# Kernel tuning notes

Measured on AMD Instinct MI355X. Metric: run time of the kernel, lower is better.

The kernel has to match this reference:

```python
import jax, jax.numpy as jnp
import numpy as np

BLOCK_SIZE = 16
MASK_TOKEN_ID = 31999
D_MODEL = 2048
N_HEADS = 16
VOCAB = 32000
NEG = -1e30


def setup_inputs() -> dict:
    key = jax.random.key(0)
    ks = jax.random.split(key, 8)
    B, S, D, V = 1, 1024, D_MODEL, VOCAB
    sd = 1.0 / np.sqrt(D)
    return {
        "input_ids": jax.random.randint(ks[0], (B, S), 0, V),
        "attention_mask": jnp.ones((B, S), dtype=jnp.float32),
        "hidden_states": jax.random.normal(ks[1], (B, S, D), dtype=jnp.float32),
        "loss_mask": jnp.ones((B, S), dtype=jnp.float32),
        "embed_table": jax.random.normal(ks[2], (V, D), dtype=jnp.float32) * 0.02,
        "Wq": jax.random.normal(ks[3], (D, D), dtype=jnp.float32) * sd,
        "Wk": jax.random.normal(ks[4], (D, D), dtype=jnp.float32) * sd,
        "Wv": jax.random.normal(ks[5], (D, D), dtype=jnp.float32) * sd,
        "Wo": jax.random.normal(ks[6], (D, D), dtype=jnp.float32) * sd,
        "lm_head_w": jax.random.normal(ks[7], (D, V), dtype=jnp.float32) * sd,
    }


def reference(input_ids, attention_mask, hidden_states, loss_mask,
              embed_table, Wq, Wk, Wv, Wo, lm_head_w):
    B, S = input_ids.shape
    bs = BLOCK_SIZE
    L = (S // bs) * bs  # effective_len
    input_ids = input_ids[:, :L]
    hidden_states = hidden_states[:, :L, :]
    loss_mask = loss_mask[:, :L]

    positions = jnp.arange(L)
    is_block_start = positions % bs == 0
    block_ids = positions // bs

    # noise input: first token of each block real, rest MASK
    noise_ids = jnp.where(is_block_start[None, :], input_ids, MASK_TOKEN_ID)
    noise_emb = embed_table[noise_ids]  # [B, L, D]

    # [L, 2L] DFlash mask: ctx kv visible if its block < q block; noise kv if same block
    ctx_vis = block_ids[None, :] < block_ids[:, None]
    noise_vis = block_ids[:, None] == block_ids[None, :]
    full_mask = jnp.concatenate([ctx_vis, noise_vis], axis=1)  # [L, 2L] bool

    # draft attention: q from noise tokens, kv over [target_hidden ; noise]
    H = N_HEADS
    hd = hidden_states.shape[-1] // H
    kv_in = jnp.concatenate([hidden_states, noise_emb], axis=1)  # [B, 2L, D]
    q = (noise_emb @ Wq).reshape(B, L, H, hd).transpose(0, 2, 1, 3)      # [B,H,L,hd]
    k = (kv_in @ Wk).reshape(B, 2 * L, H, hd).transpose(0, 2, 1, 3)      # [B,H,2L,hd]
    v = (kv_in @ Wv).reshape(B, 2 * L, H, hd).transpose(0, 2, 1, 3)
    scores = jnp.einsum("bhqd,bhkd->bhqk", q, k) / jnp.sqrt(jnp.float32(hd))
    scores = jnp.where(full_mask[None, None, :, :], scores, NEG)
    attn = jax.nn.softmax(scores, axis=-1)
    ctx = jnp.einsum("bhqk,bhkd->bhqd", attn, v)
    hidden = ctx.transpose(0, 2, 1, 3).reshape(B, L, -1) @ Wo  # [B, L, D]

    logits = hidden @ lm_head_w  # [B, L, V]

    # dflash loss mask: exclude first block and block starts (gamma=None)
    is_first_block = block_ids == 0
    valid = (~is_first_block) & (~is_block_start)
    combined = loss_mask * valid.astype(jnp.float32)  # [B, L]
    active = combined > 1e-6

    logp = jax.nn.log_softmax(logits, axis=-1)
    ce = -jnp.take_along_axis(logp, input_ids[..., None], axis=-1)[..., 0]  # [B, L]
    count = jnp.sum(active.astype(jnp.float32))
    loss = jnp.sum(jnp.where(active, ce, 0.0)) / count

    preds = jnp.argmax(logits, axis=-1)
    correct = jnp.sum(jnp.where(active, (preds == input_ids).astype(jnp.float32), 0.0))
    accuracy = correct / count
    return loss, accuracy
```

## Files before the change

### kernel.cpp

```cpp
#include <hip/hip_runtime.h>

typedef unsigned int uint32;
typedef unsigned short u16;
typedef __attribute__((ext_vector_type(8))) short bf16x8;
typedef __attribute__((ext_vector_type(4))) float f32x4;

__device__ __forceinline__ u16 f2b(float f) {
  uint32 u = __float_as_uint(f);
  u = (u + 0x7fffu + ((u >> 16) & 1u)) >> 16;
  return (u16)u;
}
__device__ __forceinline__ float b2f(u16 h) {
  return __uint_as_float(((uint32)h) << 16);
}
__device__ __forceinline__ void gl_lds16(const void* g, void* l) {
  typedef const __attribute__((address_space(1))) void* gp_t;
  typedef __attribute__((address_space(3))) void* lp_t;
  __builtin_amdgcn_global_load_lds((gp_t)g, (lp_t)l, 16, 0, 0);
}

#define L 1024
#define D 2048
#define NH 16
#define HD 128
#define VOCAB 32000
#define KV 2048
#define MASK_ID 31999

static constexpr long OFF_KV  = 0;
static constexpr long OFF_WTQ = OFF_KV  + 8388608;
static constexpr long OFF_WTK = OFF_WTQ + 8388608;
static constexpr long OFF_WTV = OFF_WTK + 8388608;
static constexpr long OFF_WTO = OFF_WTV + 8388608;
static constexpr long OFF_Q   = OFF_WTO + 8388608;
static constexpr long OFF_K   = OFF_Q   + 4194304;
static constexpr long OFF_VT  = OFF_K   + 8388608;
static constexpr long OFF_SC  = OFF_VT  + 8388608;
static constexpr long OFF_CTX = OFF_SC  + 67108864;
static constexpr long OFF_HID = OFF_CTX + 4194304;
static constexpr long OFF_LMT = OFF_HID + 4194304;
static constexpr long OFF_LOG = OFF_LMT + 131072000;
static constexpr long OFF_ROW = OFF_LOG + 65536000;
static constexpr long WS_NEED = OFF_ROW + 8192;

__global__ __launch_bounds__(256) void prep_kv(const float* __restrict__ hs,
                                               const int* __restrict__ ids,
                                               const float* __restrict__ emb,
                                               u16* __restrict__ kv) {
  int r = blockIdx.x;
  int t = threadIdx.x;
  const float* src;
  if (r < L) {
    src = hs + (long)r * D;
  } else {
    int p = r - L;
    int id = ((p & 15) == 0) ? ids[p] : MASK_ID;
    src = emb + (long)id * D;
  }
  float4 a = *(const float4*)(src + t * 8);
  float4 b = *(const float4*)(src + t * 8 + 4);
  u16* dst = kv + (long)r * D + t * 8;
  ushort4 o0, o1;
  o0.x = f2b(a.x); o0.y = f2b(a.y); o0.z = f2b(a.z); o0.w = f2b(a.w);
  o1.x = f2b(b.x); o1.y = f2b(b.y); o1.z = f2b(b.z); o1.w = f2b(b.w);
  *(ushort4*)dst = o0;
  *(ushort4*)(dst + 4) = o1;
}

__device__ __forceinline__ void transpose_body(const float* __restrict__ W,
                                               u16* __restrict__ WT,
                                               int Kd, int Nd) {
  __shared__ float tile[64][65];
  int n0 = blockIdx.x * 64;
  int k0 = blockIdx.y * 64;
  int t = threadIdx.x;
#pragma unroll
  for (int p = 0; p < 4; ++p) {
    int idx = p * 256 + t;
    int r = idx >> 4;
    int c = (idx & 15) << 2;
    float4 v = *(const float4*)(W + (long)(k0 + r) * Nd + n0 + c);
    tile[r][c] = v.x; tile[r][c + 1] = v.y; tile[r][c + 2] = v.z; tile[r][c + 3] = v.w;
  }
  __syncthreads();
#pragma unroll
  for (int p = 0; p < 4; ++p) {
    int idx = p * 256 + t;
    int rn = idx >> 4;
    int ck = (idx & 15) << 2;
    ushort4 o;
    o.x = f2b(tile[ck][rn]);
    o.y = f2b(tile[ck + 1][rn]);
    o.z = f2b(tile[ck + 2][rn]);
    o.w = f2b(tile[ck + 3][rn]);
    *(ushort4*)(WT + (long)(n0 + rn) * Kd + k0 + ck) = o;
  }
}

__global__ __launch_bounds__(256) void transpose_conv(const float* __restrict__ W,
                                                      u16* __restrict__ WT,
                                                      int Kd, int Nd) {
  transpose_body(W, WT, Kd, Nd);
}

__global__ __launch_bounds__(256) void transpose4(const float* __restrict__ W0, const float* __restrict__ W1,
                                                  const float* __restrict__ W2, const float* __restrict__ W3,
                                                  u16* __restrict__ T0, u16* __restrict__ T1,
                                                  u16* __restrict__ T2, u16* __restrict__ T3) {
  int z = blockIdx.z;
  const float* W = (z == 0) ? W0 : (z == 1) ? W1 : (z == 2) ? W2 : W3;
  u16* T = (z == 0) ? T0 : (z == 1) ? T1 : (z == 2) ? T2 : T3;
  transpose_body(W, T, D, D);
}

#define EPI_PLAIN 0
#define EPI_QKV 3

template <int EPI>
__global__ __launch_bounds__(256) void gemm128(const u16* __restrict__ A, int lda, long aHead,
                                               const u16* __restrict__ BT, int ldb, long bHead,
                                               u16* __restrict__ C, int ldc, long cHead,
                                               int Kd) {
  __shared__ __align__(16) char lds[16384];
  char* a_lds = lds;
  char* b_lds = lds + 8192;
  int tid = threadIdx.x;
  int lane = tid & 63;
  int wave = tid >> 6;
  int wr = wave >> 1, wc = wave & 1;
  int h = blockIdx.z;
  long tm = (long)blockIdx.x * 128;
  long tn = (long)blockIdx.y * 128;
  const u16* Ap = A + (long)h * aHead + tm * lda;
  const u16* Bp = BT + (long)h * bHead + tn * ldb;

  int soff = tid * 16;
  int srow = soff >> 6;
  int scol = (soff & 63) >> 1;
  char* aldsb = a_lds + wave * 1024;
  char* bldsb = b_lds + wave * 1024;

  f32x4 acc[4][4];
#pragma unroll
  for (int i = 0; i < 4; ++i)
#pragma unroll
    for (int j = 0; j < 4; ++j) acc[i][j] = (f32x4){0.f, 0.f, 0.f, 0.f};

  for (int k0 = 0; k0 < Kd; k0 += 32) {
#pragma unroll
    for (int r = 0; r < 2; ++r) {
      gl_lds16(Ap + (long)(srow + r * 64) * lda + k0 + scol, aldsb + r * 4096);
      gl_lds16(Bp + (long)(srow + r * 64) * ldb + k0 + scol, bldsb + r * 4096);
    }
    __syncthreads();
    bf16x8 af[4], bfr[4];
    int ka = (lane >> 4) << 4;
#pragma unroll
    for (int mi = 0; mi < 4; ++mi)
      af[mi] = *(const bf16x8*)(a_lds + (wr * 64 + mi * 16 + (lane & 15)) * 64 + ka);
#pragma unroll
    for (int ni = 0; ni < 4; ++ni)
      bfr[ni] = *(const bf16x8*)(b_lds + (wc * 64 + ni * 16 + (lane & 15)) * 64 + ka);
#pragma unroll
    for (int mi = 0; mi < 4; ++mi)
#pragma unroll
      for (int ni = 0; ni < 4; ++ni)
        acc[mi][ni] = __builtin_amdgcn_mfma_f32_16x16x32_bf16(af[mi], bfr[ni], acc[mi][ni], 0, 0, 0);
    __syncthreads();
  }

  long crow0 = tm + wr * 64 + ((lane >> 4) << 2);
  int ccol0 = wc * 64 + (lane & 15);
  u16* Cp = C + (long)h * cHead;
#pragma unroll
  for (int mi = 0; mi < 4; ++mi) {
#pragma unroll
    for (int ni = 0; ni < 4; ++ni) {
      long col = tn + ccol0 + ni * 16;
#pragma unroll
      for (int j = 0; j < 4; ++j) {
        long row = crow0 + mi * 16 + j;
        Cp[row * ldc + col] = f2b(acc[mi][ni][j]);
      }
    }
  }
}

template <int EPI>
__global__ __launch_bounds__(512, 2) void gemm256(const u16* __restrict__ A, int lda,
                                                  const u16* __restrict__ BT, int ldb,
                                                  u16* __restrict__ C, int ldc,
                                                  int Kd, int mtiles,
                                                  u16* __restrict__ Cq, u16* __restrict__ Ck,
                                                  u16* __restrict__ Cv) {
  __shared__ __align__(16) char lds[131072];
  int nwg = gridDim.x;
  int orig = blockIdx.x;
  int q8 = nwg >> 3, r8 = nwg & 7;
  int xcd = orig & 7, idx = orig >> 3;
  int wg = (xcd < r8 ? xcd * (q8 + 1) : r8 * (q8 + 1) + (xcd - r8) * q8) + idx;
  int tm, tn;
  if (EPI == EPI_QKV) {
    if (wg < 32) { tn = wg >> 2; tm = 4 + (wg & 3); }
    else { int e = wg - 32; tn = 8 + (e >> 3); tm = e & 7; }
  } else {
    tm = wg % mtiles; tn = wg / mtiles;
  }

  int tid = threadIdx.x, lane = tid & 63, w = tid >> 6;
  int wm = w >> 2, wn = w & 3;
  const u16* Ap = A + (long)tm * 256 * lda;
  const u16* Bp = BT + (long)tn * 256 * ldb;
  int NT = Kd >> 6;
  int maxs = NT << 2;

  auto STAGE_SLOT = [&](int s) {
    if (s >= maxs) return;
    int tau = s >> 2, hh = s & 3;
    int kind = (hh & 1) ^ 1;
    int ks = hh >> 1;
    const u16* src = kind ? Bp : Ap;
    int ld = kind ? ldb : lda;
    char* dst0 = lds + (tau & 1) * 65536 + kind * 32768 + ks * 16384;
    long kbase = (long)tau * 64 + ks * 32;
#pragma unroll
    for (int l = 0; l < 2; ++l) {
      int o = tid * 16 + l * 8192;
      int rr = o >> 6;
      int ch = (o >> 4) & 3;
      int clog = ch ^ ((rr >> 1) & 3);
      gl_lds16(src + (long)rr * ld + kbase + clog * 8, dst0 + w * 1024 + l * 8192);
    }
  };
  auto LDA = [&](int tau, int ks, int mi) -> bf16x8 {
    int rr = wm * 128 + mi * 16 + (lane & 15);
    int qq = lane >> 4;
    return *(const bf16x8*)(lds + (tau & 1) * 65536 + ks * 16384 + rr * 64 +
                            ((qq ^ ((rr >> 1) & 3)) << 4));
  };
  auto LDB = [&](int tau, int ks, int ni) -> bf16x8 {
    int rr = wn * 64 + ni * 16 + (lane & 15);
    int qq = lane >> 4;
    return *(const bf16x8*)(lds + (tau & 1) * 65536 + 32768 + ks * 16384 + rr * 64 +
                            ((qq ^ ((rr >> 1) & 3)) << 4));
  };

  f32x4 acc[8][4];
#pragma unroll
  for (int i = 0; i < 8; ++i)
#pragma unroll
    for (int j = 0; j < 4; ++j) acc[i][j] = (f32x4){0.f, 0.f, 0.f, 0.f};

  STAGE_SLOT(0); STAGE_SLOT(1); STAGE_SLOT(2); STAGE_SLOT(3);
  asm volatile("s_waitcnt vmcnt(4)" ::: "memory");
  STAGE_SLOT(4); STAGE_SLOT(5); STAGE_SLOT(6);
  asm volatile("s_waitcnt vmcnt(6)" ::: "memory");
  __builtin_amdgcn_s_barrier();
  __builtin_amdgcn_sched_barrier(0);

  bf16x8 bfr[4];

#define G256_PHASE(TAU, KS, MH, SLOT, WAITV)                                   \
  {                                                                            \
    bf16x8 af[4];                                                              \
    if (MH == 0) {                                                             \
      bfr[0] = LDB(TAU, KS, 0); bfr[1] = LDB(TAU, KS, 1);                      \
      bfr[2] = LDB(TAU, KS, 2); bfr[3] = LDB(TAU, KS, 3);                      \
    }                                                                          \
    af[0] = LDA(TAU, KS, MH * 4 + 0); af[1] = LDA(TAU, KS, MH * 4 + 1);        \
    af[2] = LDA(TAU, KS, MH * 4 + 2); af[3] = LDA(TAU, KS, MH * 4 + 3);        \
    STAGE_SLOT(SLOT);                                                          \
    __builtin_amdgcn_sched_barrier(0);                                         \
    __builtin_amdgcn_s_barrier();                                              \
    asm volatile("s_waitcnt lgkmcnt(0)" ::: "memory");                         \
    __builtin_amdgcn_sched_barrier(0);                                         \
    __builtin_amdgcn_s_setprio(1);                                             \
    _Pragma("unroll")                                                          \
    for (int mi2 = 0; mi2 < 4; ++mi2)                                          \
      _Pragma("unroll")                                                        \
      for (int ni = 0; ni < 4; ++ni)                                           \
        acc[MH * 4 + mi2][ni] = __builtin_amdgcn_mfma_f32_16x16x32_bf16(       \
            af[mi2], bfr[ni], acc[MH * 4 + mi2][ni], 0, 0, 0);                 \
    __builtin_amdgcn_s_setprio(0);                                             \
    __builtin_amdgcn_sched_barrier(0);                                         \
    if (WAITV == 6) asm volatile("s_waitcnt vmcnt(6)" ::: "memory");           \
    else if (WAITV == 0) asm volatile("s_waitcnt vmcnt(0)" ::: "memory");      \
    __builtin_amdgcn_s_barrier();                                              \
    __builtin_amdgcn_sched_barrier(0);                                         \
  }

  for (int t = 0; t < NT; t += 2) {
    int s0 = 4 * t;
    int w4 = (t + 2 >= NT) ? 0 : 6;
    G256_PHASE(t,     0, 0, s0 + 7,  -1)
    G256_PHASE(t,     0, 1, s0 + 8,  -1)
    G256_PHASE(t,     1, 0, s0 + 9,  -1)
    G256_PHASE(t,     1, 1, s0 + 10, w4)
    G256_PHASE(t + 1, 0, 0, s0 + 11, -1)
    G256_PHASE(t + 1, 0, 1, s0 + 12, -1)
    G256_PHASE(t + 1, 1, 0, s0 + 13, -1)
    G256_PHASE(t + 1, 1, 1, s0 + 14, 6)
  }
#undef G256_PHASE

  long crow = (long)tm * 256 + wm * 128 + ((lane >> 4) << 2);
  long ccol = (long)tn * 256 + wn * 64 + (lane & 15);
#pragma unroll
  for (int mi = 0; mi < 8; ++mi)
#pragma unroll
    for (int ni = 0; ni < 4; ++ni)
#pragma unroll
      for (int j = 0; j < 4; ++j) {
        long row = crow + mi * 16 + j;
        long col = ccol + ni * 16;
        u16 val = f2b(acc[mi][ni][j]);
        if (EPI == EPI_PLAIN) {
          C[row * ldc + col] = val;
        } else {
          if (col < 2048) {
            if (row >= 1024) Cq[(row - 1024) * D + col] = val;
          } else if (col < 4096) {
            Ck[row * D + (col - 2048)] = val;
          } else {
            Cv[(col - 4096) * KV + row] = val;
          }
        }
      }
}

__global__ __launch_bounds__(256) void flash_attn(const u16* __restrict__ qb,
                                                  const u16* __restrict__ kb,
                                                  const u16* __restrict__ vt,
                                                  u16* __restrict__ ctx) {
  int tid = threadIdx.x;
  int lane = tid & 63;
  int wid = blockIdx.x * 4 + (tid >> 6);
  int h = wid >> 6;
  int rb = wid & 63;
  int lq = lane & 15;
  int g = lane >> 4;
  const float scale = 0.08838834764831845f;

  const u16* qrow = qb + (long)(rb * 16 + lq) * D + h * HD + g * 8;
  bf16x8 qf[4];
#pragma unroll
  for (int c = 0; c < 4; ++c) qf[c] = *(const bf16x8*)(qrow + c * 32);

  f32x4 o[8];
#pragma unroll
  for (int i = 0; i < 8; ++i) o[i] = (f32x4){0.f, 0.f, 0.f, 0.f};
  float m = -1e30f, lsum = 0.f;

  int nb = rb + 1;
  for (int bp = 0; bp < nb; bp += 2) {
    bool validB = (bp + 1) < nb;
    int tokA = (bp < rb) ? bp * 16 : 1024 + rb * 16;
    int bB = bp + 1;
    int tokB = validB ? ((bB < rb) ? bB * 16 : 1024 + rb * 16) : tokA;

    f32x4 sA = (f32x4){0.f, 0.f, 0.f, 0.f};
    f32x4 sB = (f32x4){0.f, 0.f, 0.f, 0.f};
    const u16* ka = kb + (long)(tokA + lq) * D + h * HD + g * 8;
#pragma unroll
    for (int c = 0; c < 4; ++c) {
      bf16x8 kf = *(const bf16x8*)(ka + c * 32);
      sA = __builtin_amdgcn_mfma_f32_16x16x32_bf16(kf, qf[c], sA, 0, 0, 0);
    }
    if (validB) {
      const u16* kbp = kb + (long)(tokB + lq) * D + h * HD + g * 8;
#pragma unroll
      for (int c = 0; c < 4; ++c) {
        bf16x8 kf = *(const bf16x8*)(kbp + c * 32);
        sB = __builtin_amdgcn_mfma_f32_16x16x32_bf16(kf, qf[c], sB, 0, 0, 0);
      }
    }

    float s8[8];
#pragma unroll
    for (int j = 0; j < 4; ++j) s8[j] = sA[j] * scale;
#pragma unroll
    for (int j = 0; j < 4; ++j) s8[4 + j] = validB ? sB[j] * scale : -1e30f;
    float mx = s8[0];
#pragma unroll
    for (int j = 1; j < 8; ++j) mx = fmaxf(mx, s8[j]);
    mx = fmaxf(mx, __shfl_xor(mx, 16));
    mx = fmaxf(mx, __shfl_xor(mx, 32));
    float mn = fmaxf(m, mx);
    float sc_f = __expf(m - mn);
    m = mn;
    float p[8], ps = 0.f;
#pragma unroll
    for (int j = 0; j < 8; ++j) { p[j] = __expf(s8[j] - mn); ps += p[j]; }
    ps += __shfl_xor(ps, 16);
    ps += __shfl_xor(ps, 32);
    lsum = lsum * sc_f + ps;

    uint32 Aw0 = (uint32)f2b(p[0]) | ((uint32)f2b(p[1]) << 16);
    uint32 Aw1 = (uint32)f2b(p[2]) | ((uint32)f2b(p[3]) << 16);
    uint32 Bw0 = (uint32)f2b(p[4]) | ((uint32)f2b(p[5]) << 16);
    uint32 Bw1 = (uint32)f2b(p[6]) | ((uint32)f2b(p[7]) << 16);
    int s0 = (((2 * g) & 3) << 4) + lq;
    int s1 = (((2 * g + 1) & 3) << 4) + lq;
    uint32 a00 = (uint32)__shfl((int)Aw0, s0), a01 = (uint32)__shfl((int)Aw1, s0);
    uint32 a10 = (uint32)__shfl((int)Aw0, s1), a11 = (uint32)__shfl((int)Aw1, s1);
    uint32 b00 = (uint32)__shfl((int)Bw0, s0), b01 = (uint32)__shfl((int)Bw1, s0);
    uint32 b10 = (uint32)__shfl((int)Bw0, s1), b11 = (uint32)__shfl((int)Bw1, s1);
    union { uint32 u[4]; bf16x8 v; } pu;
    pu.u[0] = (g < 2) ? a00 : b00;
    pu.u[1] = (g < 2) ? a01 : b01;
    pu.u[2] = (g < 2) ? a10 : b10;
    pu.u[3] = (g < 2) ? a11 : b11;

#pragma unroll
    for (int nt = 0; nt < 8; ++nt)
#pragma unroll
      for (int j = 0; j < 4; ++j) o[nt][j] *= sc_f;
    int tok_g = (g < 2) ? (tokA + g * 8) : (tokB + (g - 2) * 8);
    const u16* vrow = vt + (long)(h * HD + lq) * KV + tok_g;
#pragma unroll
    for (int nt = 0; nt < 8; ++nt) {
      bf16x8 vf = *(const bf16x8*)(vrow + (long)nt * 16 * KV);
      o[nt] = __builtin_amdgcn_mfma_f32_16x16x32_bf16(vf, pu.v, o[nt], 0, 0, 0);
    }
  }

  float inv = 1.f / lsum;
  u16* cp = ctx + (long)(rb * 16 + lq) * D + h * HD + g * 4;
#pragma unroll
  for (int nt = 0; nt < 8; ++nt) {
    ushort4 st;
    st.x = f2b(o[nt][0] * inv); st.y = f2b(o[nt][1] * inv);
    st.z = f2b(o[nt][2] * inv); st.w = f2b(o[nt][3] * inv);
    *(ushort4*)(cp + nt * 16) = st;
  }
}

__global__ __launch_bounds__(256) void row_ce(const u16* __restrict__ logits,
                                              const int* __restrict__ ids,
                                              float* __restrict__ rowbuf) {
  int row = blockIdx.x;
  const u16* p = logits + (long)row * VOCAB;
  int t = threadIdx.x;
  int lane = t & 63, w = t >> 6;
  float m = -1e30f;
  int am = VOCAB;
  for (int i = t * 8; i < VOCAB; i += 2048) {
    bf16x8 v = *(const bf16x8*)(p + i);
#pragma unroll
    for (int j = 0; j < 8; ++j) {
      float f = b2f((u16)v[j]);
      if (f > m) { m = f; am = i + j; }
      else if (f == m && (i + j) < am) am = i + j;
    }
  }
  for (int off = 1; off < 64; off <<= 1) {
    float om = __shfl_xor(m, off);
    int oa = __shfl_xor(am, off);
    if (om > m || (om == m && oa < am)) { m = om; am = oa; }
  }
  __shared__ float smax[4]; __shared__ int sidx[4]; __shared__ float ssum[4];
  if (lane == 0) { smax[w] = m; sidx[w] = am; }
  __syncthreads();
  float gm = smax[0]; int gi = sidx[0];
#pragma unroll
  for (int q = 1; q < 4; ++q) {
    if (smax[q] > gm || (smax[q] == gm && sidx[q] < gi)) { gm = smax[q]; gi = sidx[q]; }
  }
  float s = 0.f;
  for (int i = t * 8; i < VOCAB; i += 2048) {
    bf16x8 v = *(const bf16x8*)(p + i);
#pragma unroll
    for (int j = 0; j < 8; ++j) s += __expf(b2f((u16)v[j]) - gm);
  }
  for (int off = 1; off < 64; off <<= 1) s += __shfl_xor(s, off);
  if (lane == 0) ssum[w] = s;
  __syncthreads();
  if (t == 0) {
    float gs = ssum[0] + ssum[1] + ssum[2] + ssum[3];
    int tgt = ids[row];
    float tl = b2f(p[tgt]);
    rowbuf[row * 2] = gm + logf(gs) - tl;
    rowbuf[row * 2 + 1] = (gi == tgt) ? 1.f : 0.f;
  }
}

__global__ __launch_bounds__(256) void final_reduce(const float* __restrict__ rowbuf,
                                                    const float* __restrict__ loss_mask,
                                                    float* __restrict__ out) {
  int t = threadIdx.x;
  float ce = 0.f, cnt = 0.f, cor = 0.f;
  for (int r = t; r < L; r += 256) {
    bool valid = (r >= 16) && ((r & 15) != 0);
    float comb = loss_mask[r] * (valid ? 1.f : 0.f);
    if (comb > 1e-6f) {
      ce += rowbuf[r * 2];
      cor += rowbuf[r * 2 + 1];
      cnt += 1.f;
    }
  }
  for (int off = 1; off < 64; off <<= 1) {
    ce += __shfl_xor(ce, off);
    cnt += __shfl_xor(cnt, off);
    cor += __shfl_xor(cor, off);
  }
  __shared__ float s1[4], s2[4], s3[4];
  int lane = t & 63, w = t >> 6;
  if (lane == 0) { s1[w] = ce; s2[w] = cnt; s3[w] = cor; }
  __syncthreads();
  if (t == 0) {
    float C = s1[0] + s1[1] + s1[2] + s1[3];
    float N = s2[0] + s2[1] + s2[2] + s2[3];
    float R = s3[0] + s3[1] + s3[2] + s3[3];
    out[0] = C / N;
    out[1] = R / N;
  }
}

__global__ void ws_too_small(float* out, float mb) {
  if (threadIdx.x == 0) { out[0] = 1e6f + mb; out[1] = -1e6f; }
}

extern "C" void kernel_launch(void* const* d_in, const int* in_sizes, int n_in,
                              void* d_out, int out_size, void* d_ws, size_t ws_size,
                              hipStream_t stream) {
  const int* ids = (const int*)d_in[0];
  const float* hs = (const float*)d_in[2];
  const float* lmask = (const float*)d_in[3];
  const float* emb = (const float*)d_in[4];
  const float* Wq = (const float*)d_in[5];
  const float* Wk = (const float*)d_in[6];
  const float* Wv = (const float*)d_in[7];
  const float* Wo = (const float*)d_in[8];
  const float* Wlm = (const float*)d_in[9];
  float* out = (float*)d_out;
  char* ws = (char*)d_ws;

  if (ws_size < (size_t)WS_NEED) {
    ws_too_small<<<1, 64, 0, stream>>>(out, (float)(ws_size >> 20));
    return;
  }

  u16* kv  = (u16*)(ws + OFF_KV);
  u16* wtq = (u16*)(ws + OFF_WTQ);
  u16* wtk = (u16*)(ws + OFF_WTK);
  u16* wtv = (u16*)(ws + OFF_WTV);
  u16* wto = (u16*)(ws + OFF_WTO);
  u16* qb  = (u16*)(ws + OFF_Q);
  u16* kb  = (u16*)(ws + OFF_K);
  u16* vt  = (u16*)(ws + OFF_VT);
  u16* ctx = (u16*)(ws + OFF_CTX);
  u16* hid = (u16*)(ws + OFF_HID);
  u16* lmt = (u16*)(ws + OFF_LMT);
  u16* lgt = (u16*)(ws + OFF_LOG);
  float* rowbuf = (float*)(ws + OFF_ROW);

  prep_kv<<<2048, 256, 0, stream>>>(hs, ids, emb, kv);
  transpose4<<<dim3(32, 32, 4), 256, 0, stream>>>(Wq, Wk, Wv, Wo, wtq, wtk, wtv, wto);
  transpose_conv<<<dim3(500, 32), 256, 0, stream>>>(Wlm, lmt, D, VOCAB);

  gemm256<EPI_QKV><<<dim3(160), 512, 0, stream>>>(kv, D, wtq, D, nullptr, 0, D, 0,
                                                  qb, kb, vt);

  flash_attn<<<dim3(256), 256, 0, stream>>>(qb, kb, vt, ctx);

  gemm128<EPI_PLAIN><<<dim3(8, 16, 1), 256, 0, stream>>>(ctx, D, 0, wto, D, 0, hid, D, 0, D);
  gemm256<EPI_PLAIN><<<dim3(500), 512, 0, stream>>>(hid, D, lmt, D, lgt, VOCAB, D, 4,
                                                    nullptr, nullptr, nullptr);

  row_ce<<<1024, 256, 0, stream>>>(lgt, ids, rowbuf);
  final_reduce<<<1, 256, 0, stream>>>(rowbuf, lmask, out);
}
```

Before: 458.5 us.

## Fuse cross-entropy partials into LM-head GEMM epilogue, enlarge transpose tiles, balance attention

The LM-head GEMM now reduces each 256x256 output tile to per-row partial max, sum-exp, argmax and target logit instead of writing the bf16 logits. A small combine kernel merges the 125 partials per row, so the full logits write and re-read and the row_ce kernel are gone. Separately, the weight transpose kernels use 128x128 tiles with a larger LDS buffer, and flash attention pairs early and late row blocks per workgroup to balance causal work. One risk is that the fused softmax uses fp32 accumulators rather than bf16-rounded logits, which slightly changes numerics. The larger transpose tile also raises LDS use per block.

```diff
diff --git a/kernel.cpp b/kernel.cpp
--- a/kernel.cpp
+++ b/kernel.cpp
@@ -35,12 +35,14 @@
 static constexpr long OFF_Q   = OFF_WTO + 8388608;
 static constexpr long OFF_K   = OFF_Q   + 4194304;
 static constexpr long OFF_VT  = OFF_K   + 8388608;
-static constexpr long OFF_SC  = OFF_VT  + 8388608;
-static constexpr long OFF_CTX = OFF_SC  + 67108864;
+static constexpr long OFF_CTX = OFF_VT  + 8388608;
 static constexpr long OFF_HID = OFF_CTX + 4194304;
 static constexpr long OFF_LMT = OFF_HID + 4194304;
-static constexpr long OFF_LOG = OFF_LMT + 131072000;
-static constexpr long OFF_ROW = OFF_LOG + 65536000;
+static constexpr long OFF_PM  = OFF_LMT + 131072000;
+static constexpr long OFF_PS  = OFF_PM  + 524288;
+static constexpr long OFF_PI  = OFF_PS  + 524288;
+static constexpr long OFF_PT  = OFF_PI  + 524288;
+static constexpr long OFF_ROW = OFF_PT  + 4096;
 static constexpr long WS_NEED = OFF_ROW + 8192;
 
 __global__ __launch_bounds__(256) void prep_kv(const float* __restrict__ hs,
@@ -70,30 +72,29 @@
 __device__ __forceinline__ void transpose_body(const float* __restrict__ W,
                                                u16* __restrict__ WT,
                                                int Kd, int Nd) {
-  __shared__ float tile[64][65];
-  int n0 = blockIdx.x * 64;
-  int k0 = blockIdx.y * 64;
+  __shared__ float tile[128 * 129];
+  int n0 = blockIdx.x * 128;
+  int k0 = blockIdx.y * 128;
   int t = threadIdx.x;
-#pragma unroll
-  for (int p = 0; p < 4; ++p) {
-    int idx = p * 256 + t;
-    int r = idx >> 4;
-    int c = (idx & 15) << 2;
-    float4 v = *(const float4*)(W + (long)(k0 + r) * Nd + n0 + c);
-    tile[r][c] = v.x; tile[r][c + 1] = v.y; tile[r][c + 2] = v.z; tile[r][c + 3] = v.w;
+  int r = t >> 5;
+  int c4 = (t & 31) * 4;
+#pragma unroll
+  for (int p = 0; p < 16; ++p) {
+    int kk = p * 8 + r;
+    float4 v = *(const float4*)(W + (long)(k0 + kk) * Nd + n0 + c4);
+    float* dst = tile + kk * 129 + c4;
+    dst[0] = v.x; dst[1] = v.y; dst[2] = v.z; dst[3] = v.w;
   }
   __syncthreads();
 #pragma unroll
-  for (int p = 0; p < 4; ++p) {
-    int idx = p * 256 + t;
-    int rn = idx >> 4;
-    int ck = (idx & 15) << 2;
+  for (int p = 0; p < 16; ++p) {
+    int nn = p * 8 + r;
     ushort4 o;
-    o.x = f2b(tile[ck][rn]);
-    o.y = f2b(tile[ck + 1][rn]);
-    o.z = f2b(tile[ck + 2][rn]);
-    o.w = f2b(tile[ck + 3][rn]);
-    *(ushort4*)(WT + (long)(n0 + rn) * Kd + k0 + ck) = o;
+    o.x = f2b(tile[(c4 + 0) * 129 + nn]);
+    o.y = f2b(tile[(c4 + 1) * 129 + nn]);
+    o.z = f2b(tile[(c4 + 2) * 129 + nn]);
+    o.w = f2b(tile[(c4 + 3) * 129 + nn]);
+    *(ushort4*)(WT + (long)(n0 + nn) * Kd + k0 + c4) = o;
   }
 }
 
@@ -115,6 +116,7 @@
 
 #define EPI_PLAIN 0
 #define EPI_QKV 3
+#define EPI_CE 4
 
 template <int EPI>
 __global__ __launch_bounds__(256) void gemm128(const u16* __restrict__ A, int lda, long aHead,
@@ -192,7 +194,12 @@
                                                   u16* __restrict__ C, int ldc,
                                                   int Kd, int mtiles,
                                                   u16* __restrict__ Cq, u16* __restrict__ Ck,
-                                                  u16* __restrict__ Cv) {
+                                                  u16* __restrict__ Cv,
+                                                  const int* __restrict__ ids,
+                                                  float* __restrict__ PMAX,
+                                                  float* __restrict__ PSUM,
+                                                  int* __restrict__ PARGI,
+                                                  float* __restrict__ PTGT) {
   __shared__ __align__(16) char lds[131072];
   int nwg = gridDim.x;
   int orig = blockIdx.x;
@@ -303,6 +310,67 @@
   }
 #undef G256_PHASE
 
+  if (EPI == EPI_CE) {
+    __syncthreads();
+    float* smax = (float*)lds;
+    float* ssum = smax + 1024;
+    int* sargi = (int*)(ssum + 1024);
+    int lq = lane & 15, qq = lane >> 4;
+#pragma unroll
+    for (int mi = 0; mi < 8; ++mi) {
+#pragma unroll
+      for (int j = 0; j < 4; ++j) {
+        int lrow = mi * 16 + qq * 4 + j;
+        long grow = (long)tm * 256 + wm * 128 + lrow;
+        int tgt = ids[grow];
+        float v[4];
+        float mx = -1e30f; int ai = 0;
+#pragma unroll
+        for (int ni = 0; ni < 4; ++ni) {
+          v[ni] = acc[mi][ni][j];
+          int col = tn * 256 + wn * 64 + ni * 16 + lq;
+          if (col == tgt) PTGT[grow] = v[ni];
+          if (v[ni] > mx) { mx = v[ni]; ai = col; }
+        }
+#pragma unroll
+        for (int off = 1; off < 16; off <<= 1) {
+          float om = __shfl_xor(mx, off);
+          int oa = __shfl_xor(ai, off);
+          if (om > mx || (om == mx && oa < ai)) { mx = om; ai = oa; }
+        }
+        float se = 0.f;
+#pragma unroll
+        for (int ni = 0; ni < 4; ++ni) se += __expf(v[ni] - mx);
+#pragma unroll
+        for (int off = 1; off < 16; off <<= 1) se += __shfl_xor(se, off);
+        if (lq == 0) {
+          int f = wm * 128 + lrow;
+          smax[f * 4 + wn] = mx;
+          ssum[f * 4 + wn] = se;
+          sargi[f * 4 + wn] = ai;
+        }
+      }
+    }
+    __syncthreads();
+    if (lane < 32) {
+      int f = w * 32 + lane;
+      float m_t = smax[f * 4]; int a_t = sargi[f * 4];
+#pragma unroll
+      for (int x = 1; x < 4; ++x) {
+        float om = smax[f * 4 + x]; int oa = sargi[f * 4 + x];
+        if (om > m_t || (om == m_t && oa < a_t)) { m_t = om; a_t = oa; }
+      }
+      float s_t = 0.f;
+#pragma unroll
+      for (int x = 0; x < 4; ++x) s_t += ssum[f * 4 + x] * __expf(smax[f * 4 + x] - m_t);
+      long grow = (long)tm * 256 + f;
+      PMAX[grow * 128 + tn] = m_t;
+      PSUM[grow * 128 + tn] = s_t;
+      PARGI[grow * 128 + tn] = a_t;
+    }
+    return;
+  }
+
   long crow = (long)tm * 256 + wm * 128 + ((lane >> 4) << 2);
   long ccol = (long)tn * 256 + wn * 64 + (lane & 15);
 #pragma unroll
@@ -328,6 +396,38 @@
       }
 }
 
+__global__ __launch_bounds__(256) void ce_combine(const float* __restrict__ PMAX,
+                                                  const float* __restrict__ PSUM,
+                                                  const int* __restrict__ PARGI,
+                                                  const float* __restrict__ PTGT,
+                                                  const int* __restrict__ ids,
+                                                  float* __restrict__ rowbuf) {
+  int row = blockIdx.x * 4 + (threadIdx.x >> 6);
+  int lane = threadIdx.x & 63;
+  const float* pm = PMAX + (long)row * 128;
+  const float* ps = PSUM + (long)row * 128;
+  const int* pi = PARGI + (long)row * 128;
+  float m0 = (lane < 125) ? pm[lane] : -1e30f;
+  int a0 = (lane < 125) ? pi[lane] : (1 << 30);
+  float m1 = (lane + 64 < 125) ? pm[lane + 64] : -1e30f;
+  int a1 = (lane + 64 < 125) ? pi[lane + 64] : (1 << 30);
+  float mg = m0; int ag = a0;
+  if (m1 > mg || (m1 == mg && a1 < ag)) { mg = m1; ag = a1; }
+  for (int off = 1; off < 64; off <<= 1) {
+    float om = __shfl_xor(mg, off);
+    int oa = __shfl_xor(ag, off);
+    if (om > mg || (om == mg && oa < ag)) { mg = om; ag = oa; }
+  }
+  float s = 0.f;
+  if (lane < 125) s += ps[lane] * __expf(m0 - mg);
+  if (lane + 64 < 125) s += ps[lane + 64] * __expf(m1 - mg);
+  for (int off = 1; off < 64; off <<= 1) s += __shfl_xor(s, off);
+  if (lane == 0) {
+    rowbuf[row * 2] = mg + logf(s) - PTGT[row];
+    rowbuf[row * 2 + 1] = (ag == ids[row]) ? 1.f : 0.f;
+  }
+}
+
 __global__ __launch_bounds__(256) void flash_attn(const u16* __restrict__ qb,
                                                   const u16* __restrict__ kb,
                                                   const u16* __restrict__ vt,
@@ -335,8 +435,10 @@
   int tid = threadIdx.x;
   int lane = tid & 63;
   int wid = blockIdx.x * 4 + (tid >> 6);
-  int h = wid >> 6;
-  int rb = wid & 63;
+  int pairid = wid >> 1;
+  int h = pairid >> 5;
+  int pr = pairid & 31;
+  int rb = (wid & 1) ? (63 - pr) : pr;
   int lq = lane & 15;
   int g = lane >> 4;
   const float scale = 0.08838834764831845f;
@@ -435,55 +537,6 @@
   }
 }
 
-__global__ __launch_bounds__(256) void row_ce(const u16* __restrict__ logits,
-                                              const int* __restrict__ ids,
-                                              float* __restrict__ rowbuf) {
-  int row = blockIdx.x;
-  const u16* p = logits + (long)row * VOCAB;
-  int t = threadIdx.x;
-  int lane = t & 63, w = t >> 6;
-  float m = -1e30f;
-  int am = VOCAB;
-  for (int i = t * 8; i < VOCAB; i += 2048) {
-    bf16x8 v = *(const bf16x8*)(p + i);
-#pragma unroll
-    for (int j = 0; j < 8; ++j) {
-      float f = b2f((u16)v[j]);
-      if (f > m) { m = f; am = i + j; }
-      else if (f == m && (i + j) < am) am = i + j;
-    }
-  }
-  for (int off = 1; off < 64; off <<= 1) {
-    float om = __shfl_xor(m, off);
-    int oa = __shfl_xor(am, off);
-    if (om > m || (om == m && oa < am)) { m = om; am = oa; }
-  }
-  __shared__ float smax[4]; __shared__ int sidx[4]; __shared__ float ssum[4];
-  if (lane == 0) { smax[w] = m; sidx[w] = am; }
-  __syncthreads();
-  float gm = smax[0]; int gi = sidx[0];
-#pragma unroll
-  for (int q = 1; q < 4; ++q) {
-    if (smax[q] > gm || (smax[q] == gm && sidx[q] < gi)) { gm = smax[q]; gi = sidx[q]; }
-  }
-  float s = 0.f;
-  for (int i = t * 8; i < VOCAB; i += 2048) {
-    bf16x8 v = *(const bf16x8*)(p + i);
-#pragma unroll
-    for (int j = 0; j < 8; ++j) s += __expf(b2f((u16)v[j]) - gm);
-  }
-  for (int off = 1; off < 64; off <<= 1) s += __shfl_xor(s, off);
-  if (lane == 0) ssum[w] = s;
-  __syncthreads();
-  if (t == 0) {
-    float gs = ssum[0] + ssum[1] + ssum[2] + ssum[3];
-    int tgt = ids[row];
-    float tl = b2f(p[tgt]);
-    rowbuf[row * 2] = gm + logf(gs) - tl;
-    rowbuf[row * 2 + 1] = (gi == tgt) ? 1.f : 0.f;
-  }
-}
-
 __global__ __launch_bounds__(256) void final_reduce(const float* __restrict__ rowbuf,
                                                     const float* __restrict__ loss_mask,
                                                     float* __restrict__ out) {
@@ -551,22 +604,28 @@
   u16* ctx = (u16*)(ws + OFF_CTX);
   u16* hid = (u16*)(ws + OFF_HID);
   u16* lmt = (u16*)(ws + OFF_LMT);
-  u16* lgt = (u16*)(ws + OFF_LOG);
+  float* PMAX = (float*)(ws + OFF_PM);
+  float* PSUM = (float*)(ws + OFF_PS);
+  int* PARGI = (int*)(ws + OFF_PI);
+  float* PTGT = (float*)(ws + OFF_PT);
   float* rowbuf = (float*)(ws + OFF_ROW);
 
   prep_kv<<<2048, 256, 0, stream>>>(hs, ids, emb, kv);
-  transpose4<<<dim3(32, 32, 4), 256, 0, stream>>>(Wq, Wk, Wv, Wo, wtq, wtk, wtv, wto);
-  transpose_conv<<<dim3(500, 32), 256, 0, stream>>>(Wlm, lmt, D, VOCAB);
+  transpose4<<<dim3(16, 16, 4), 256, 0, stream>>>(Wq, Wk, Wv, Wo, wtq, wtk, wtv, wto);
+  transpose_conv<<<dim3(250, 16), 256, 0, stream>>>(Wlm, lmt, D, VOCAB);
 
   gemm256<EPI_QKV><<<dim3(160), 512, 0, stream>>>(kv, D, wtq, D, nullptr, 0, D, 0,
-                                                  qb, kb, vt);
+                                                  qb, kb, vt,
+                                                  nullptr, nullptr, nullptr, nullptr, nullptr);
 
   flash_attn<<<dim3(256), 256, 0, stream>>>(qb, kb, vt, ctx);
 
   gemm128<EPI_PLAIN><<<dim3(8, 16, 1), 256, 0, stream>>>(ctx, D, 0, wto, D, 0, hid, D, 0, D);
-  gemm256<EPI_PLAIN><<<dim3(500), 512, 0, stream>>>(hid, D, lmt, D, lgt, VOCAB, D, 4,
-                                                    nullptr, nullptr, nullptr);
-
-  row_ce<<<1024, 256, 0, stream>>>(lgt, ids, rowbuf);
+
+  gemm256<EPI_CE><<<dim3(500), 512, 0, stream>>>(hid, D, lmt, D, nullptr, 0, D, 4,
+                                                 nullptr, nullptr, nullptr,
+                                                 ids, PMAX, PSUM, PARGI, PTGT);
+
+  ce_combine<<<256, 256, 0, stream>>>(PMAX, PSUM, PARGI, PTGT, ids, rowbuf);
   final_reduce<<<1, 256, 0, stream>>>(rowbuf, lmask, out);
 }
```

After: 465.3 us. Within noise of the previous version (+1.5%).
